# Kernel tuning notes

Hardware: AMD Instinct MI355X
Metric: run time of the kernel (lower is better)

Reference implementation:

```python
import jax, jax.numpy as jnp
import numpy as np

NUM_GRAPHS = 512  # batch_size (number of segments)


def setup_inputs() -> dict:
    key = jax.random.key(0)
    k1, k2 = jax.random.split(key)
    x = jax.random.normal(k1, (200000, 256), dtype=jnp.float32)
    batch = jnp.sort(jax.random.randint(k2, (200000,), 0, NUM_GRAPHS, dtype=jnp.int64))
    return {"x": x, "batch": batch}


def reference(x, batch):
    # scatter-add node features into per-graph sums: out[g] = sum_{i: batch[i]==g} x[i]
    return jax.ops.segment_sum(x, batch, num_segments=NUM_GRAPHS)
```

## Files before the change

### kernel.cpp

```cpp
#include <hip/hip_runtime.h>


#define FEAT 256
#define F4   (FEAT / 4)
#define NSEG 512

__global__ void seg_bounds_kernel(const int* __restrict__ batch,
                                  int* __restrict__ start, int n) {
    int r = blockIdx.x * blockDim.x + threadIdx.x;
    if (r >= n) return;
    int cur = batch[r];
    if (r == 0) {
        for (int g = 0; g <= cur; ++g) start[g] = 0;
    } else {
        int prev = batch[r - 1];
        for (int g = prev + 1; g <= cur; ++g) start[g] = r;
    }
    if (r == n - 1) {
        for (int g = cur + 1; g <= NSEG; ++g) start[g] = n;
    }
}

__global__ __launch_bounds__(256) void GraphAddPooling_39539468927441_kernel(
    const float* __restrict__ x, const int* __restrict__ start,
    float* __restrict__ out)
{
    const int g    = blockIdx.x;
    const int lane = threadIdx.x & 63;
    const int wave = threadIdx.x >> 6;

    const int r0 = start[g];
    const int r1 = start[g + 1];

    const float4* __restrict__ x4 = (const float4*)x;

    float4 a0 = make_float4(0.f, 0.f, 0.f, 0.f);
    float4 a1 = a0, a2 = a0, a3 = a0;

    int r = r0 + wave;
    for (; r + 12 < r1; r += 16) {
        float4 v0 = x4[(size_t)r        * F4 + lane];
        float4 v1 = x4[(size_t)(r + 4)  * F4 + lane];
        float4 v2 = x4[(size_t)(r + 8)  * F4 + lane];
        float4 v3 = x4[(size_t)(r + 12) * F4 + lane];
        a0.x += v0.x; a0.y += v0.y; a0.z += v0.z; a0.w += v0.w;
        a1.x += v1.x; a1.y += v1.y; a1.z += v1.z; a1.w += v1.w;
        a2.x += v2.x; a2.y += v2.y; a2.z += v2.z; a2.w += v2.w;
        a3.x += v3.x; a3.y += v3.y; a3.z += v3.z; a3.w += v3.w;
    }
    for (; r < r1; r += 4) {
        float4 v = x4[(size_t)r * F4 + lane];
        a0.x += v.x; a0.y += v.y; a0.z += v.z; a0.w += v.w;
    }
    a0.x += a1.x + a2.x + a3.x;
    a0.y += a1.y + a2.y + a3.y;
    a0.z += a1.z + a2.z + a3.z;
    a0.w += a1.w + a2.w + a3.w;

    __shared__ float4 red[4][F4];
    red[wave][lane] = a0;
    __syncthreads();
    if (wave == 0) {
        float4 s = red[0][lane];
        float4 b = red[1][lane], c = red[2][lane], d = red[3][lane];
        s.x += b.x + c.x + d.x;
        s.y += b.y + c.y + d.y;
        s.z += b.z + c.z + d.z;
        s.w += b.w + c.w + d.w;
        ((float4*)out)[(size_t)g * F4 + lane] = s;
    }
}

extern "C" void kernel_launch(void* const* d_in, const int* in_sizes, int n_in,
                              void* d_out, int out_size, void* d_ws, size_t ws_size,
                              hipStream_t stream) {
    const float* x     = (const float*)d_in[0];
    const int*   batch = (const int*)d_in[1];
    float*       out   = (float*)d_out;
    int*         start = (int*)d_ws;

    const int n_rows = in_sizes[1];

    seg_bounds_kernel<<<(n_rows + 255) / 256, 256, 0, stream>>>(batch, start, n_rows);
    GraphAddPooling_39539468927441_kernel<<<NSEG, 256, 0, stream>>>(x, start, out);
}
```

Baseline: 281.7 us.

## Replace segment-bounds kernel with in-block wave-parallel binary search

Removes the separate seg_bounds_kernel launch and workspace array. Each block instead finds its segment's start and end rows with a 64-way wave-cooperative search over the sorted batch array, using ballot and popcount, before summing rows. This saves one kernel launch and a global round-trip, at the cost of a few dependent global-memory search steps at the start of every block.

```diff
diff --git a/kernel.cpp b/kernel.cpp
--- a/kernel.cpp
+++ b/kernel.cpp
@@ -5,32 +5,44 @@
 #define F4   (FEAT / 4)
 #define NSEG 512
 
-__global__ void seg_bounds_kernel(const int* __restrict__ batch,
-                                  int* __restrict__ start, int n) {
-    int r = blockIdx.x * blockDim.x + threadIdx.x;
-    if (r >= n) return;
-    int cur = batch[r];
-    if (r == 0) {
-        for (int g = 0; g <= cur; ++g) start[g] = 0;
-    } else {
-        int prev = batch[r - 1];
-        for (int g = prev + 1; g <= cur; ++g) start[g] = r;
+__device__ __forceinline__ int lower_bound_wave(const int* __restrict__ batch,
+                                                int n, int target, int lane) {
+    int lo = 0, len = n;
+    while (len > 64) {
+        int step = len >> 6;
+        int q    = lo + lane * step;
+        unsigned long long m = __ballot(batch[q] < target);
+        int c = __popcll(m);
+        if (c == 0) return lo;
+        int nlo = lo + (c - 1) * step + 1;
+        int nhi = (c < 64) ? (lo + c * step)
+                           : (lo + len);
+        lo  = nlo;
+        len = nhi - nlo;
     }
-    if (r == n - 1) {
-        for (int g = cur + 1; g <= NSEG; ++g) start[g] = n;
+    if (len > 0) {
+        bool cond = (lane < len) && (batch[lo + lane] < target);
+        lo += __popcll(__ballot(cond));
     }
+    return lo;
 }
 
 __global__ __launch_bounds__(256) void GraphAddPooling_39539468927441_kernel(
-    const float* __restrict__ x, const int* __restrict__ start,
-    float* __restrict__ out)
+    const float* __restrict__ x, const int* __restrict__ batch,
+    float* __restrict__ out, int n)
 {
     const int g    = blockIdx.x;
     const int lane = threadIdx.x & 63;
     const int wave = threadIdx.x >> 6;
 
-    const int r0 = start[g];
-    const int r1 = start[g + 1];
+    __shared__ int sb[2];
+    if (wave < 2) {
+        int b = lower_bound_wave(batch, n, g + wave, lane);
+        if (lane == 0) sb[wave] = b;
+    }
+    __syncthreads();
+    const int r0 = sb[0];
+    const int r1 = sb[1];
 
     const float4* __restrict__ x4 = (const float4*)x;
 
@@ -77,10 +89,8 @@
     const float* x     = (const float*)d_in[0];
     const int*   batch = (const int*)d_in[1];
     float*       out   = (float*)d_out;
-    int*         start = (int*)d_ws;
 
     const int n_rows = in_sizes[1];
 
-    seg_bounds_kernel<<<(n_rows + 255) / 256, 256, 0, stream>>>(batch, start, n_rows);
-    GraphAddPooling_39539468927441_kernel<<<NSEG, 256, 0, stream>>>(x, start, out);
+    GraphAddPooling_39539468927441_kernel<<<NSEG, 256, 0, stream>>>(x, batch, out, n_rows);
 }
```

After: 280.5 us, median of 2. No clear change (-0.4%).

## Split rows evenly across blocks and merge segment partials with atomics

Applied to the files above, without the earlier changes.

Replaces the segment-boundary kernel plus one-block-per-segment reduction with a single kernel in which 2048 blocks each take an equal contiguous row range. Each wave walks its rows, accumulates while the segment id stays the same, and flushes partial sums into the output with float atomicAdd when the segment changes. The output is zeroed with a memset first. This removes the extra boundary pass and the load imbalance from uneven segment sizes, and gives more blocks for latency hiding. In exchange it adds atomic traffic and per-row segment-id loads, and the summation order becomes nondeterministic.

```diff
diff --git a/kernel.cpp b/kernel.cpp
--- a/kernel.cpp
+++ b/kernel.cpp
@@ -4,71 +4,70 @@
 #define FEAT 256
 #define F4   (FEAT / 4)
 #define NSEG 512
+#define GRID 2048
 
-__global__ void seg_bounds_kernel(const int* __restrict__ batch,
-                                  int* __restrict__ start, int n) {
-    int r = blockIdx.x * blockDim.x + threadIdx.x;
-    if (r >= n) return;
-    int cur = batch[r];
-    if (r == 0) {
-        for (int g = 0; g <= cur; ++g) start[g] = 0;
-    } else {
-        int prev = batch[r - 1];
-        for (int g = prev + 1; g <= cur; ++g) start[g] = r;
-    }
-    if (r == n - 1) {
-        for (int g = cur + 1; g <= NSEG; ++g) start[g] = n;
-    }
+__device__ __forceinline__ void flush_acc(float* __restrict__ out, int seg,
+                                          int lane, const float4& a) {
+    float* p = out + (size_t)seg * FEAT + lane * 4;
+    atomicAdd(p + 0, a.x);
+    atomicAdd(p + 1, a.y);
+    atomicAdd(p + 2, a.z);
+    atomicAdd(p + 3, a.w);
 }
 
 __global__ __launch_bounds__(256) void GraphAddPooling_39539468927441_kernel(
-    const float* __restrict__ x, const int* __restrict__ start,
-    float* __restrict__ out)
+    const float* __restrict__ x, const int* __restrict__ batch,
+    float* __restrict__ out, int n)
 {
-    const int g    = blockIdx.x;
     const int lane = threadIdx.x & 63;
     const int wave = threadIdx.x >> 6;
+    const int b    = blockIdx.x;
 
-    const int r0 = start[g];
-    const int r1 = start[g + 1];
+    const int c0 = (int)(((long long)n * b) / GRID);
+    const int c1 = (int)(((long long)n * (b + 1)) / GRID);
+    const int len = c1 - c0;
+    const int w0 = c0 + (len * wave) / 4;
+    const int w1 = c0 + (len * (wave + 1)) / 4;
+    if (w0 >= w1) return;
 
     const float4* __restrict__ x4 = (const float4*)x;
 
-    float4 a0 = make_float4(0.f, 0.f, 0.f, 0.f);
-    float4 a1 = a0, a2 = a0, a3 = a0;
+    int cur = batch[w0];
+    float4 acc = make_float4(0.f, 0.f, 0.f, 0.f);
 
-    int r = r0 + wave;
-    for (; r + 12 < r1; r += 16) {
-        float4 v0 = x4[(size_t)r        * F4 + lane];
-        float4 v1 = x4[(size_t)(r + 4)  * F4 + lane];
-        float4 v2 = x4[(size_t)(r + 8)  * F4 + lane];
-        float4 v3 = x4[(size_t)(r + 12) * F4 + lane];
-        a0.x += v0.x; a0.y += v0.y; a0.z += v0.z; a0.w += v0.w;
-        a1.x += v1.x; a1.y += v1.y; a1.z += v1.z; a1.w += v1.w;
-        a2.x += v2.x; a2.y += v2.y; a2.z += v2.z; a2.w += v2.w;
-        a3.x += v3.x; a3.y += v3.y; a3.z += v3.z; a3.w += v3.w;
+    int r = w0;
+    for (; r + 3 < w1; r += 4) {
+        float4 v0 = x4[(size_t)(r + 0) * F4 + lane];
+        float4 v1 = x4[(size_t)(r + 1) * F4 + lane];
+        float4 v2 = x4[(size_t)(r + 2) * F4 + lane];
+        float4 v3 = x4[(size_t)(r + 3) * F4 + lane];
+        int s0 = batch[r];
+        int s3 = batch[r + 3];
+        if (s0 == cur && s3 == cur) {
+            acc.x += v0.x + v1.x + v2.x + v3.x;
+            acc.y += v0.y + v1.y + v2.y + v3.y;
+            acc.z += v0.z + v1.z + v2.z + v3.z;
+            acc.w += v0.w + v1.w + v2.w + v3.w;
+        } else {
+            int s1 = batch[r + 1];
+            int s2 = batch[r + 2];
+            if (s0 != cur) { flush_acc(out, cur, lane, acc); acc = make_float4(0,0,0,0); cur = s0; }
+            acc.x += v0.x; acc.y += v0.y; acc.z += v0.z; acc.w += v0.w;
+            if (s1 != cur) { flush_acc(out, cur, lane, acc); acc = make_float4(0,0,0,0); cur = s1; }
+            acc.x += v1.x; acc.y += v1.y; acc.z += v1.z; acc.w += v1.w;
+            if (s2 != cur) { flush_acc(out, cur, lane, acc); acc = make_float4(0,0,0,0); cur = s2; }
+            acc.x += v2.x; acc.y += v2.y; acc.z += v2.z; acc.w += v2.w;
+            if (s3 != cur) { flush_acc(out, cur, lane, acc); acc = make_float4(0,0,0,0); cur = s3; }
+            acc.x += v3.x; acc.y += v3.y; acc.z += v3.z; acc.w += v3.w;
+        }
     }
-    for (; r < r1; r += 4) {
+    for (; r < w1; ++r) {
         float4 v = x4[(size_t)r * F4 + lane];
-        a0.x += v.x; a0.y += v.y; a0.z += v.z; a0.w += v.w;
+        int s = batch[r];
+        if (s != cur) { flush_acc(out, cur, lane, acc); acc = make_float4(0,0,0,0); cur = s; }
+        acc.x += v.x; acc.y += v.y; acc.z += v.z; acc.w += v.w;
     }
-    a0.x += a1.x + a2.x + a3.x;
-    a0.y += a1.y + a2.y + a3.y;
-    a0.z += a1.z + a2.z + a3.z;
-    a0.w += a1.w + a2.w + a3.w;
-
-    __shared__ float4 red[4][F4];
-    red[wave][lane] = a0;
-    __syncthreads();
-    if (wave == 0) {
-        float4 s = red[0][lane];
-        float4 b = red[1][lane], c = red[2][lane], d = red[3][lane];
-        s.x += b.x + c.x + d.x;
-        s.y += b.y + c.y + d.y;
-        s.z += b.z + c.z + d.z;
-        s.w += b.w + c.w + d.w;
-        ((float4*)out)[(size_t)g * F4 + lane] = s;
-    }
+    flush_acc(out, cur, lane, acc);
 }
 
 extern "C" void kernel_launch(void* const* d_in, const int* in_sizes, int n_in,
@@ -77,10 +76,9 @@
     const float* x     = (const float*)d_in[0];
     const int*   batch = (const int*)d_in[1];
     float*       out   = (float*)d_out;
-    int*         start = (int*)d_ws;
 
     const int n_rows = in_sizes[1];
 
-    seg_bounds_kernel<<<(n_rows + 255) / 256, 256, 0, stream>>>(batch, start, n_rows);
-    GraphAddPooling_39539468927441_kernel<<<NSEG, 256, 0, stream>>>(x, start, out);
+    hipMemsetAsync(out, 0, out_size, stream);
+    GraphAddPooling_39539468927441_kernel<<<GRID, 256, 0, stream>>>(x, batch, out, n_rows);
 }
```

After: 284.3 us. About the same (+0.9%).
